# Kernel tuning notes

Hardware: AMD Instinct MI355X
Metric: run time of the kernel (lower is better)

Reference implementation:

```python
import jax, jax.numpy as jnp
import numpy as np

TEMPERATURE = 0.07
BASE_TEMPERATURE = 0.07
EPS = 0.0001  # matches the +0.0001 in the torch code


def _l2norm(x):
    return x / jnp.clip(jnp.linalg.norm(x, axis=-1, keepdims=True), 1e-12, None)


def setup_inputs() -> dict:
    key = jax.random.key(0)
    k1, k2, k3 = jax.random.split(key, 3)
    # Sampled hard anchors: [total_classes=102, n_view=10, d=256], unit-norm
    # (original normalizes feats with F.normalize before _hard_anchor_sampling).
    X_anchor = _l2norm(jax.random.normal(k1, (102, 10, 256), dtype=jnp.float32))
    y_anchor = jax.random.randint(k2, (102,), 0, 19)
    # Memory queue of negatives: [class_num=19, cache_size=5000, d=256], unit-norm.
    queue = _l2norm(jax.random.normal(k3, (19, 5000, 256), dtype=jnp.float32))
    return {"X_anchor": X_anchor, "y_anchor": y_anchor, "queue": queue}


def reference(X_anchor, y_anchor, queue):
    anchor_num, n_view, d = X_anchor.shape
    class_num, cache_size, _ = queue.shape

    # anchor_feature = cat(unbind(X_anchor, dim=1), dim=0)  -> view-major order [n_view*anchor_num, d]
    anchor_feature = jnp.transpose(X_anchor, (1, 0, 2)).reshape(n_view * anchor_num, d)
    # _sample_negative flattens the queue class-major: [class_num*cache_size, d]
    contrast_feature = queue.reshape(class_num * cache_size, d)

    # mask = eq(y_anchor, y_contrast.T) then .repeat(anchor_count=n_view, contrast_count=1)
    y_a = jnp.tile(y_anchor, n_view)                                  # [N]
    y_c = jnp.repeat(jnp.arange(class_num, dtype=y_anchor.dtype), cache_size)  # [M]
    mask = (y_a[:, None] == y_c[None, :]).astype(X_anchor.dtype)      # [N, M]

    logits = jnp.matmul(anchor_feature, contrast_feature.T) / TEMPERATURE  # [N, M]
    logits_max = jax.lax.stop_gradient(jnp.max(logits, axis=1, keepdims=True))
    logits = logits - logits_max

    exp_logits = jnp.exp(logits)
    neg_sum = jnp.sum(exp_logits * (1.0 - mask), axis=1, keepdims=True)  # [N, 1]
    log_prob = logits - jnp.log(exp_logits + neg_sum)

    mean_log_prob_pos = jnp.sum(mask * log_prob, axis=1) / (jnp.sum(mask, axis=1) + EPS)
    loss = -(TEMPERATURE / BASE_TEMPERATURE) * mean_log_prob_pos
    return jnp.mean(loss)
```

## Files before the change

### kernel.cpp

```cpp
#include <hip/hip_runtime.h>
#include <hip/hip_bf16.h>
#include <stdint.h>

#define NCLS   19
#define CACHE  5000
#define NTILE  313
#define DDIM   256
#define NANCH  102
#define NVIEW  10
#define NROWS  1020
#define NSUB   13
#define NCHUNK (NCLS*NSUB)
#define NWG    (4*NCHUNK)
#define SCALE_A 20.6099319733f
#define LN2     0.69314718056f

using bf16x8 = __attribute__((ext_vector_type(8))) __bf16;
using f32x4  = __attribute__((ext_vector_type(4))) float;

#if __has_builtin(__builtin_amdgcn_exp2f)
#define EXP2(x) __builtin_amdgcn_exp2f(x)
#else
#define EXP2(x) __expf((x) * LN2)
#endif

static __device__ __forceinline__ unsigned short f2bf(float x) {
    unsigned int u = __float_as_uint(x);
    unsigned int r = (u + 0x7FFFu + ((u >> 16) & 1u)) >> 16;
    return (unsigned short)r;
}

__global__ __launch_bounds__(256) void conv_anchor2(const float* __restrict__ X,
                                                    unsigned short* __restrict__ Abf) {
    int n = blockIdx.x;
    int k = threadIdx.x;
    float v = 0.f;
    if (n < NROWS) {
        int vv = n / NANCH, a = n - vv * NANCH;
        v = X[((size_t)a * NVIEW + vv) * DDIM + k] * SCALE_A;
    }
    Abf[(size_t)n * DDIM + k] = f2bf(v);
}

__global__ __launch_bounds__(256, 2) void pass1_kernel(
    const unsigned short* __restrict__ Abf, const float* __restrict__ Qf,
    const int* __restrict__ y,
    float* __restrict__ Pt, float* __restrict__ Pe, float* __restrict__ Ps)
{
    __shared__ unsigned char lds[2][8192];

    int orig = blockIdx.x;
    int xcd = orig & 7, slot = orig >> 3;
    int wid = (xcd < 4 ? xcd * 124 : 496 + (xcd - 4) * 123) + slot;
    int rt = wid & 3;
    int cs = wid >> 2;
    int cls = cs / NSUB;
    int sub = cs - cls * NSUB;
    int t0 = (NTILE * sub) / NSUB, t1 = (NTILE * (sub + 1)) / NSUB;

    int tid = threadIdx.x;
    int wave = tid >> 6, lane = tid & 63;
    int lg = lane >> 4, lm = lane & 15;
    int wrb = rt * 256 + wave * 64;

    int c   = tid >> 4;
    int seg = tid & 15;
    int skk = seg >> 1;
    int sidx0 = skk * 64 + ((seg & 1) * 2) * 16 + c;
    unsigned sb0 = (unsigned)(sidx0 * 16) ^ (unsigned)(skk << 4);
    unsigned sb1 = (unsigned)((sidx0 + 16) * 16) ^ (unsigned)(skk << 4);
    const float* qbase = Qf + (size_t)cls * CACHE * DDIM + seg * 16;

    bf16x8 afrag[4][8];
    #pragma unroll
    for (int f = 0; f < 4; ++f)
        #pragma unroll
        for (int kk = 0; kk < 8; ++kk)
            afrag[f][kk] = *reinterpret_cast<const bf16x8*>(
                Abf + (size_t)(wrb + f * 16 + lm) * DDIM + kk * 32 + lg * 8);

    float tacc[4][4] = {}, sacc[4][4] = {};

#define SLOAD(t) do {                                                         \
        int _col = (t) * 16 + c;                                              \
        s_ok = _col < CACHE;                                                  \
        const f32x4* _src = reinterpret_cast<const f32x4*>(                   \
            qbase + (size_t)(s_ok ? _col : CACHE - 1) * DDIM);                \
        s_r0 = _src[0]; s_r1 = _src[1]; s_r2 = _src[2]; s_r3 = _src[3];       \
    } while (0)

#define CVTWRITE(buf) do {                                                    \
        bf16x8 _p0, _p1;                                                      \
        _Pragma("unroll")                                                     \
        for (int j = 0; j < 4; ++j) {                                         \
            _p0[j]     = (__bf16)s_r0[j];                                     \
            _p0[j + 4] = (__bf16)s_r1[j];                                     \
            _p1[j]     = (__bf16)s_r2[j];                                     \
            _p1[j + 4] = (__bf16)s_r3[j];                                     \
        }                                                                     \
        bf16x8 _z = {};                                                       \
        if (!s_ok) { _p0 = _z; _p1 = _z; }                                    \
        *reinterpret_cast<bf16x8*>(&lds[buf][sb0]) = _p0;                     \
        *reinterpret_cast<bf16x8*>(&lds[buf][sb1]) = _p1;                     \
    } while (0)

#define COMPUTE(buf) do {                                                     \
        bf16x8 bfrag[8];                                                      \
        _Pragma("unroll")                                                     \
        for (int kk = 0; kk < 8; ++kk)                                        \
            bfrag[kk] = *reinterpret_cast<const bf16x8*>(                     \
                &lds[buf][(unsigned)((kk * 64 + lane) * 16) ^ (unsigned)(kk << 4)]); \
        f32x4 acc[4];                                                         \
        _Pragma("unroll")                                                     \
        for (int f = 0; f < 4; ++f) acc[f] = (f32x4){0.f, 0.f, 0.f, 0.f};     \
        _Pragma("unroll")                                                     \
        for (int kk = 0; kk < 8; ++kk)                                        \
            _Pragma("unroll")                                                 \
            for (int f = 0; f < 4; ++f)                                       \
                acc[f] = __builtin_amdgcn_mfma_f32_16x16x32_bf16(             \
                    afrag[f][kk], bfrag[kk], acc[f], 0, 0, 0);                \
        _Pragma("unroll")                                                     \
        for (int f = 0; f < 4; ++f)                                           \
            _Pragma("unroll")                                                 \
            for (int r = 0; r < 4; ++r) {                                     \
                float v = acc[f][r];                         \
                tacc[f][r] += EXP2(v);              \
                sacc[f][r] += v;                                              \
            }                                                                 \
    } while (0)

    f32x4 s_r0, s_r1, s_r2, s_r3;
    bool s_ok;
    int nt = t1 - t0;

    SLOAD(t0);
    CVTWRITE(0);
    __syncthreads();

    int cur = 0;
    for (int it = 0; it < nt; ++it) {
        if (it + 1 < nt) SLOAD(t0 + it + 1);
        COMPUTE(cur);
        if (it + 1 < nt) CVTWRITE(cur ^ 1);
        __syncthreads();
        cur ^= 1;
    }
#undef SLOAD
#undef CVTWRITE
#undef COMPUTE

    #pragma unroll
    for (int f = 0; f < 4; ++f)
        #pragma unroll
        for (int r = 0; r < 4; ++r) {
            float t = tacc[f][r], s = sacc[f][r];
            #pragma unroll
            for (int m = 1; m < 16; m <<= 1) {
                t += __shfl_xor(t, m);
                s += __shfl_xor(s, m);
            }
            if (lm == 0) {
                int row = wrb + f * 16 + lg * 4 + r;
                float mp = (row < NROWS && y[row % NANCH] == cls) ? 1.0f : 0.0f;
                size_t idx = (size_t)cs * 1024 + row;
                Pt[idx] = t; Pe[idx] = mp * t; Ps[idx] = mp * s;
            }
        }
}

__global__ __launch_bounds__(256) void reduce_rows(const float* __restrict__ Pt,
                                                   const float* __restrict__ Pe,
                                                   const float* __restrict__ Ps,
                                                   float* __restrict__ rowloss) {
    int tid = threadIdx.x;
    int row = blockIdx.x * 64 + (tid >> 2);
    int part = tid & 3;
    float tot = 0.f, pe = 0.f, ps = 0.f;
    for (int c = part; c < NCHUNK; c += 4) {
        size_t idx = (size_t)c * 1024 + row;
        tot += Pt[idx]; pe += Pe[idx]; ps += Ps[idx];
    }
    tot += __shfl_xor(tot, 1); pe += __shfl_xor(pe, 1); ps += __shfl_xor(ps, 1);
    tot += __shfl_xor(tot, 2); pe += __shfl_xor(pe, 2); ps += __shfl_xor(ps, 2);
    if (part == 0) {
        float r = 0.f;
        if (row < NROWS) {
            float ns    = tot - pe - 144.0f;
            float pos_e = pe - 8.0f;
            float pos_s = ps * LN2;
            float sum_logprob = pos_s - (5000.0f * logf(ns) + pos_e / ns);
            r = -sum_logprob / (5000.0f + 1e-4f);
        }
        rowloss[row] = r;
    }
}

__global__ __launch_bounds__(256) void pass3_kernel(const float* __restrict__ rowloss,
                                                    float* __restrict__ out) {
    float local = 0.f;
    for (int n = threadIdx.x; n < 1024; n += 256) local += rowloss[n];
    #pragma unroll
    for (int m = 1; m < 64; m <<= 1) local += __shfl_xor(local, m);
    __shared__ float sb[4];
    if ((threadIdx.x & 63) == 0) sb[threadIdx.x >> 6] = local;
    __syncthreads();
    if (threadIdx.x == 0)
        out[0] = (sb[0] + sb[1] + sb[2] + sb[3]) * (1.0f / (float)NROWS);
}

extern "C" void kernel_launch(void* const* d_in, const int* in_sizes, int n_in,
                              void* d_out, int out_size, void* d_ws, size_t ws_size,
                              hipStream_t stream) {
    const float* X  = (const float*)d_in[0];
    const int*   y  = (const int*)d_in[1];
    const float* Qf = (const float*)d_in[2];
    float* out = (float*)d_out;

    char* ws = (char*)d_ws;
    unsigned short* Abf = (unsigned short*)(ws);
    float* Pt      = (float*)(ws + 524288);
    float* Pe      = (float*)(ws + 1536000);
    float* Ps      = (float*)(ws + 2547712);
    float* rowloss = (float*)(ws + 3559424);

    conv_anchor2<<<1024, 256, 0, stream>>>(X, Abf);
    pass1_kernel<<<NWG, 256, 0, stream>>>(Abf, Qf, y, Pt, Pe, Ps);
    reduce_rows<<<16, 256, 0, stream>>>(Pt, Pe, Ps, rowloss);
    pass3_kernel<<<1, 256, 0, stream>>>(rowloss, out);
}
```

Before: 103.3 us.

## Split anchor rows into 8 row tiles per chunk and simplify LDS layout

Doubles the workgroup count by splitting the 1024 anchor rows into 8 tiles of 128 rather than 4 of 256. Each wave now holds 2 A fragments instead of 4, which cuts register pressure enough to raise launch bounds to 3 workgroups per SIMD. The staging thread mapping is changed to row-major, and the XOR-swizzled LDS layout is dropped in favour of plain offsets. The aim is more occupancy and parallelism to hide latency, at the cost of each queue tile being loaded and converted twice as often and possible LDS bank conflicts.

```diff
diff --git a/kernel.cpp b/kernel.cpp
--- a/kernel.cpp
+++ b/kernel.cpp
@@ -11,7 +11,7 @@
 #define NROWS  1020
 #define NSUB   13
 #define NCHUNK (NCLS*NSUB)
-#define NWG    (4*NCHUNK)
+#define NWG    (8*NCHUNK)
 #define SCALE_A 20.6099319733f
 #define LN2     0.69314718056f
 
@@ -42,7 +42,7 @@
     Abf[(size_t)n * DDIM + k] = f2bf(v);
 }
 
-__global__ __launch_bounds__(256, 2) void pass1_kernel(
+__global__ __launch_bounds__(256, 3) void pass1_kernel(
     const unsigned short* __restrict__ Abf, const float* __restrict__ Qf,
     const int* __restrict__ y,
     float* __restrict__ Pt, float* __restrict__ Pe, float* __restrict__ Ps)
@@ -51,9 +51,9 @@
 
     int orig = blockIdx.x;
     int xcd = orig & 7, slot = orig >> 3;
-    int wid = (xcd < 4 ? xcd * 124 : 496 + (xcd - 4) * 123) + slot;
-    int rt = wid & 3;
-    int cs = wid >> 2;
+    int wid = xcd * 247 + slot;
+    int rt = wid & 7;
+    int cs = wid >> 3;
     int cls = cs / NSUB;
     int sub = cs - cls * NSUB;
     int t0 = (NTILE * sub) / NSUB, t1 = (NTILE * (sub + 1)) / NSUB;
@@ -61,25 +61,21 @@
     int tid = threadIdx.x;
     int wave = tid >> 6, lane = tid & 63;
     int lg = lane >> 4, lm = lane & 15;
-    int wrb = rt * 256 + wave * 64;
-
-    int c   = tid >> 4;
-    int seg = tid & 15;
-    int skk = seg >> 1;
-    int sidx0 = skk * 64 + ((seg & 1) * 2) * 16 + c;
-    unsigned sb0 = (unsigned)(sidx0 * 16) ^ (unsigned)(skk << 4);
-    unsigned sb1 = (unsigned)((sidx0 + 16) * 16) ^ (unsigned)(skk << 4);
-    const float* qbase = Qf + (size_t)cls * CACHE * DDIM + seg * 16;
-
-    bf16x8 afrag[4][8];
+    int wrb = rt * 128 + wave * 32;
+
+    int c = tid & 15, r = tid >> 4;
+    unsigned wb0 = (unsigned)((r >> 1) * 1024 + (r & 1) * 512 + c * 16);
+    const float* qbase = Qf + (size_t)cls * CACHE * DDIM + r * 16;
+
+    bf16x8 afrag[2][8];
     #pragma unroll
-    for (int f = 0; f < 4; ++f)
+    for (int f = 0; f < 2; ++f)
         #pragma unroll
         for (int kk = 0; kk < 8; ++kk)
             afrag[f][kk] = *reinterpret_cast<const bf16x8*>(
                 Abf + (size_t)(wrb + f * 16 + lm) * DDIM + kk * 32 + lg * 8);
 
-    float tacc[4][4] = {}, sacc[4][4] = {};
+    float tacc[2][4] = {}, sacc[2][4] = {};
 
 #define SLOAD(t) do {                                                         \
         int _col = (t) * 16 + c;                                              \
@@ -100,8 +96,8 @@
         }                                                                     \
         bf16x8 _z = {};                                                       \
         if (!s_ok) { _p0 = _z; _p1 = _z; }                                    \
-        *reinterpret_cast<bf16x8*>(&lds[buf][sb0]) = _p0;                     \
-        *reinterpret_cast<bf16x8*>(&lds[buf][sb1]) = _p1;                     \
+        *reinterpret_cast<bf16x8*>(&lds[buf][wb0])       = _p0;               \
+        *reinterpret_cast<bf16x8*>(&lds[buf][wb0 + 256]) = _p1;               \
     } while (0)
 
 #define COMPUTE(buf) do {                                                     \
@@ -109,24 +105,21 @@
         _Pragma("unroll")                                                     \
         for (int kk = 0; kk < 8; ++kk)                                        \
             bfrag[kk] = *reinterpret_cast<const bf16x8*>(                     \
-                &lds[buf][(unsigned)((kk * 64 + lane) * 16) ^ (unsigned)(kk << 4)]); \
-        f32x4 acc[4];                                                         \
-        _Pragma("unroll")                                                     \
-        for (int f = 0; f < 4; ++f) acc[f] = (f32x4){0.f, 0.f, 0.f, 0.f};     \
-        _Pragma("unroll")                                                     \
-        for (int kk = 0; kk < 8; ++kk)                                        \
-            _Pragma("unroll")                                                 \
-            for (int f = 0; f < 4; ++f)                                       \
-                acc[f] = __builtin_amdgcn_mfma_f32_16x16x32_bf16(             \
-                    afrag[f][kk], bfrag[kk], acc[f], 0, 0, 0);                \
-        _Pragma("unroll")                                                     \
-        for (int f = 0; f < 4; ++f)                                           \
-            _Pragma("unroll")                                                 \
-            for (int r = 0; r < 4; ++r) {                                     \
-                float v = acc[f][r];                         \
-                tacc[f][r] += EXP2(v);              \
-                sacc[f][r] += v;                                              \
-            }                                                                 \
+                &lds[buf][(kk * 64 + lane) * 16]);                            \
+        f32x4 acc0 = {0.f,0.f,0.f,0.f}, acc1 = {0.f,0.f,0.f,0.f};             \
+        _Pragma("unroll")                                                     \
+        for (int kk = 0; kk < 8; ++kk) {                                      \
+            acc0 = __builtin_amdgcn_mfma_f32_16x16x32_bf16(                   \
+                afrag[0][kk], bfrag[kk], acc0, 0, 0, 0);                      \
+            acc1 = __builtin_amdgcn_mfma_f32_16x16x32_bf16(                   \
+                afrag[1][kk], bfrag[kk], acc1, 0, 0, 0);                      \
+        }                                                                     \
+        _Pragma("unroll")                                                     \
+        for (int r_ = 0; r_ < 4; ++r_) {                                      \
+            float v0 = acc0[r_], v1 = acc1[r_];                               \
+            tacc[0][r_] += EXP2(v0);  sacc[0][r_] += v0;                      \
+            tacc[1][r_] += EXP2(v1);  sacc[1][r_] += v1;                      \
+        }                                                                     \
     } while (0)
 
     f32x4 s_r0, s_r1, s_r2, s_r3;
@@ -150,17 +143,17 @@
 #undef COMPUTE
 
     #pragma unroll
-    for (int f = 0; f < 4; ++f)
+    for (int f = 0; f < 2; ++f)
         #pragma unroll
-        for (int r = 0; r < 4; ++r) {
-            float t = tacc[f][r], s = sacc[f][r];
+        for (int r_ = 0; r_ < 4; ++r_) {
+            float t = tacc[f][r_], s = sacc[f][r_];
             #pragma unroll
             for (int m = 1; m < 16; m <<= 1) {
                 t += __shfl_xor(t, m);
                 s += __shfl_xor(s, m);
             }
             if (lm == 0) {
-                int row = wrb + f * 16 + lg * 4 + r;
+                int row = wrb + f * 16 + lg * 4 + r_;
                 float mp = (row < NROWS && y[row % NANCH] == cls) ? 1.0f : 0.0f;
                 size_t idx = (size_t)cs * 1024 + row;
                 Pt[idx] = t; Pe[idx] = mp * t; Ps[idx] = mp * s;
```

New measurement: 142.9 us. 38.3% more time.

## Compute positive logit sums via class column-sums and use 512-thread workgroups

Applied to the files above, without the earlier changes.

Removes the per-element accumulation of raw logits in the main GEMM loop. The positive-logit sum is now computed algebraically as the dot product of each anchor row with its class's column sum of queue vectors, accumulated during staging and combined in a new small kernel. Workgroups grow to 512 threads covering 512 rows, which halves the grid and the number of times each queue tile is reloaded from global memory. The LDS swizzle is dropped, which may introduce bank conflicts. The colsum is taken over fp32 values rather than bf16, so rounding differs slightly from before.

```diff
diff --git a/kernel.cpp b/kernel.cpp
--- a/kernel.cpp
+++ b/kernel.cpp
@@ -11,7 +11,7 @@
 #define NROWS  1020
 #define NSUB   13
 #define NCHUNK (NCLS*NSUB)
-#define NWG    (4*NCHUNK)
+#define NWG    (2*NCHUNK)
 #define SCALE_A 20.6099319733f
 #define LN2     0.69314718056f
 
@@ -42,18 +42,18 @@
     Abf[(size_t)n * DDIM + k] = f2bf(v);
 }
 
-__global__ __launch_bounds__(256, 2) void pass1_kernel(
+__global__ __launch_bounds__(512, 1) void pass1_kernel(
     const unsigned short* __restrict__ Abf, const float* __restrict__ Qf,
     const int* __restrict__ y,
-    float* __restrict__ Pt, float* __restrict__ Pe, float* __restrict__ Ps)
+    float* __restrict__ Pt, float* __restrict__ Pe, float* __restrict__ Pcs)
 {
     __shared__ unsigned char lds[2][8192];
 
     int orig = blockIdx.x;
     int xcd = orig & 7, slot = orig >> 3;
-    int wid = (xcd < 4 ? xcd * 124 : 496 + (xcd - 4) * 123) + slot;
-    int rt = wid & 3;
-    int cs = wid >> 2;
+    int wid = (xcd < 6 ? xcd * 62 : 372 + (xcd - 6) * 61) + slot;
+    int rt = wid & 1;
+    int cs = wid >> 1;
     int cls = cs / NSUB;
     int sub = cs - cls * NSUB;
     int t0 = (NTILE * sub) / NSUB, t1 = (NTILE * (sub + 1)) / NSUB;
@@ -61,15 +61,13 @@
     int tid = threadIdx.x;
     int wave = tid >> 6, lane = tid & 63;
     int lg = lane >> 4, lm = lane & 15;
-    int wrb = rt * 256 + wave * 64;
-
-    int c   = tid >> 4;
-    int seg = tid & 15;
-    int skk = seg >> 1;
-    int sidx0 = skk * 64 + ((seg & 1) * 2) * 16 + c;
-    unsigned sb0 = (unsigned)(sidx0 * 16) ^ (unsigned)(skk << 4);
-    unsigned sb1 = (unsigned)((sidx0 + 16) * 16) ^ (unsigned)(skk << 4);
-    const float* qbase = Qf + (size_t)cls * CACHE * DDIM + seg * 16;
+    int wrb = rt * 512 + wave * 64;
+
+    int c = tid & 15, r = tid >> 4;
+    unsigned wb = (unsigned)(((r >> 2) * 64 + (r & 3) * 16 + c) * 16);
+    const float* qbase = Qf + (size_t)cls * CACHE * DDIM + r * 8;
+    bool docs = (rt == 0);
+    float csum[8] = {};
 
     bf16x8 afrag[4][8];
     #pragma unroll
@@ -79,29 +77,34 @@
             afrag[f][kk] = *reinterpret_cast<const bf16x8*>(
                 Abf + (size_t)(wrb + f * 16 + lm) * DDIM + kk * 32 + lg * 8);
 
-    float tacc[4][4] = {}, sacc[4][4] = {};
+    float tacc[4][4] = {};
 
 #define SLOAD(t) do {                                                         \
         int _col = (t) * 16 + c;                                              \
         s_ok = _col < CACHE;                                                  \
         const f32x4* _src = reinterpret_cast<const f32x4*>(                   \
             qbase + (size_t)(s_ok ? _col : CACHE - 1) * DDIM);                \
-        s_r0 = _src[0]; s_r1 = _src[1]; s_r2 = _src[2]; s_r3 = _src[3];       \
+        s_r0 = _src[0]; s_r1 = _src[1];                                       \
     } while (0)
 
 #define CVTWRITE(buf) do {                                                    \
-        bf16x8 _p0, _p1;                                                      \
+        bf16x8 _p;                                                            \
         _Pragma("unroll")                                                     \
         for (int j = 0; j < 4; ++j) {                                         \
-            _p0[j]     = (__bf16)s_r0[j];                                     \
-            _p0[j + 4] = (__bf16)s_r1[j];                                     \
-            _p1[j]     = (__bf16)s_r2[j];                                     \
-            _p1[j + 4] = (__bf16)s_r3[j];                                     \
+            _p[j]     = (__bf16)s_r0[j];                                      \
+            _p[j + 4] = (__bf16)s_r1[j];                                      \
         }                                                                     \
-        bf16x8 _z = {};                                                       \
-        if (!s_ok) { _p0 = _z; _p1 = _z; }                                    \
-        *reinterpret_cast<bf16x8*>(&lds[buf][sb0]) = _p0;                     \
-        *reinterpret_cast<bf16x8*>(&lds[buf][sb1]) = _p1;                     \
+        if (!s_ok) {                                                          \
+            bf16x8 _z = {};                                                   \
+            _p = _z;                                                          \
+        } else if (docs) {                                                    \
+            _Pragma("unroll")                                                 \
+            for (int j = 0; j < 4; ++j) {                                     \
+                csum[j]     += s_r0[j];                                       \
+                csum[j + 4] += s_r1[j];                                       \
+            }                                                                 \
+        }                                                                     \
+        *reinterpret_cast<bf16x8*>(&lds[buf][wb]) = _p;                       \
     } while (0)
 
 #define COMPUTE(buf) do {                                                     \
@@ -109,7 +112,7 @@
         _Pragma("unroll")                                                     \
         for (int kk = 0; kk < 8; ++kk)                                        \
             bfrag[kk] = *reinterpret_cast<const bf16x8*>(                     \
-                &lds[buf][(unsigned)((kk * 64 + lane) * 16) ^ (unsigned)(kk << 4)]); \
+                &lds[buf][(kk * 64 + lane) * 16]);                            \
         f32x4 acc[4];                                                         \
         _Pragma("unroll")                                                     \
         for (int f = 0; f < 4; ++f) acc[f] = (f32x4){0.f, 0.f, 0.f, 0.f};     \
@@ -122,14 +125,11 @@
         _Pragma("unroll")                                                     \
         for (int f = 0; f < 4; ++f)                                           \
             _Pragma("unroll")                                                 \
-            for (int r = 0; r < 4; ++r) {                                     \
-                float v = acc[f][r];                         \
-                tacc[f][r] += EXP2(v);              \
-                sacc[f][r] += v;                                              \
-            }                                                                 \
+            for (int r_ = 0; r_ < 4; ++r_)                                    \
+                tacc[f][r_] += EXP2(acc[f][r_]);    \
     } while (0)
 
-    f32x4 s_r0, s_r1, s_r2, s_r3;
+    f32x4 s_r0, s_r1;
     bool s_ok;
     int nt = t1 - t0;
 
@@ -152,46 +152,82 @@
     #pragma unroll
     for (int f = 0; f < 4; ++f)
         #pragma unroll
-        for (int r = 0; r < 4; ++r) {
-            float t = tacc[f][r], s = sacc[f][r];
+        for (int r_ = 0; r_ < 4; ++r_) {
+            float t = tacc[f][r_];
             #pragma unroll
-            for (int m = 1; m < 16; m <<= 1) {
-                t += __shfl_xor(t, m);
-                s += __shfl_xor(s, m);
-            }
+            for (int m = 1; m < 16; m <<= 1) t += __shfl_xor(t, m);
             if (lm == 0) {
-                int row = wrb + f * 16 + lg * 4 + r;
+                int row = wrb + f * 16 + lg * 4 + r_;
                 float mp = (row < NROWS && y[row % NANCH] == cls) ? 1.0f : 0.0f;
                 size_t idx = (size_t)cs * 1024 + row;
-                Pt[idx] = t; Pe[idx] = mp * t; Ps[idx] = mp * s;
+                Pt[idx] = t; Pe[idx] = mp * t;
             }
         }
+
+    if (docs) {
+        #pragma unroll
+        for (int j = 0; j < 8; ++j) {
+            float v = csum[j];
+            v += __shfl_xor(v, 1);
+            v += __shfl_xor(v, 2);
+            v += __shfl_xor(v, 4);
+            v += __shfl_xor(v, 8);
+            if (c == 0) Pcs[(size_t)cs * DDIM + r * 8 + j] = v;
+        }
+    }
+}
+
+__global__ __launch_bounds__(256) void colsum_combine(const float* __restrict__ Pcs,
+                                                      float* __restrict__ colsum) {
+    int cls = blockIdx.x, k = threadIdx.x;
+    float s = 0.f;
+    for (int sub = 0; sub < NSUB; ++sub)
+        s += Pcs[(size_t)(cls * NSUB + sub) * DDIM + k];
+    colsum[cls * DDIM + k] = s;
 }
 
 __global__ __launch_bounds__(256) void reduce_rows(const float* __restrict__ Pt,
                                                    const float* __restrict__ Pe,
-                                                   const float* __restrict__ Ps,
+                                                   const float* __restrict__ colsum,
+                                                   const unsigned short* __restrict__ Abf,
+                                                   const int* __restrict__ y,
                                                    float* __restrict__ rowloss) {
     int tid = threadIdx.x;
     int row = blockIdx.x * 64 + (tid >> 2);
     int part = tid & 3;
-    float tot = 0.f, pe = 0.f, ps = 0.f;
-    for (int c = part; c < NCHUNK; c += 4) {
-        size_t idx = (size_t)c * 1024 + row;
-        tot += Pt[idx]; pe += Pe[idx]; ps += Ps[idx];
-    }
-    tot += __shfl_xor(tot, 1); pe += __shfl_xor(pe, 1); ps += __shfl_xor(ps, 1);
-    tot += __shfl_xor(tot, 2); pe += __shfl_xor(pe, 2); ps += __shfl_xor(ps, 2);
+    float tot = 0.f, pe = 0.f;
+    for (int cc = part; cc < NCHUNK; cc += 4) {
+        size_t idx = (size_t)cc * 1024 + row;
+        tot += Pt[idx]; pe += Pe[idx];
+    }
+    float psd = 0.f;
+    if (row < NROWS) {
+        int cls = y[row % NANCH];
+        const bf16x8* arow = reinterpret_cast<const bf16x8*>(
+            Abf + (size_t)row * DDIM) + part * 8;
+        const f32x4* csp = reinterpret_cast<const f32x4*>(
+            colsum + cls * DDIM + part * 64);
+        #pragma unroll
+        for (int i = 0; i < 8; ++i) {
+            bf16x8 av = arow[i];
+            f32x4 c0 = csp[i * 2], c1 = csp[i * 2 + 1];
+            #pragma unroll
+            for (int j = 0; j < 4; ++j)
+                psd += (float)av[j] * c0[j] + (float)av[j + 4] * c1[j];
+        }
+    }
+    tot += __shfl_xor(tot, 1); pe += __shfl_xor(pe, 1); psd += __shfl_xor(psd, 1);
+    tot += __shfl_xor(tot, 2); pe += __shfl_xor(pe, 2); psd += __shfl_xor(psd, 2);
     if (part == 0) {
-        float r = 0.f;
+        float rl = 0.f;
         if (row < NROWS) {
             float ns    = tot - pe - 144.0f;
             float pos_e = pe - 8.0f;
-            float pos_s = ps * LN2;
+            float pos_s = psd * LN2;
             float sum_logprob = pos_s - (5000.0f * logf(ns) + pos_e / ns);
-            r = -sum_logprob / (5000.0f + 1e-4f);
-        }
-        rowloss[row] = r;
+            rl = -sum_logprob / (5000.0f + 1e-4f);
+        }
+        rowloss[row] = rl;
     }
 }
 
@@ -220,11 +256,13 @@
     unsigned short* Abf = (unsigned short*)(ws);
     float* Pt      = (float*)(ws + 524288);
     float* Pe      = (float*)(ws + 1536000);
-    float* Ps      = (float*)(ws + 2547712);
-    float* rowloss = (float*)(ws + 3559424);
+    float* Pcs     = (float*)(ws + 2547712);
+    float* colsum  = (float*)(ws + 2800640);
+    float* rowloss = (float*)(ws + 2820096);
 
     conv_anchor2<<<1024, 256, 0, stream>>>(X, Abf);
-    pass1_kernel<<<NWG, 256, 0, stream>>>(Abf, Qf, y, Pt, Pe, Ps);
-    reduce_rows<<<16, 256, 0, stream>>>(Pt, Pe, Ps, rowloss);
+    pass1_kernel<<<NWG, 512, 0, stream>>>(Abf, Qf, y, Pt, Pe, Pcs);
+    colsum_combine<<<NCLS, 256, 0, stream>>>(Pcs, colsum);
+    reduce_rows<<<16, 256, 0, stream>>>(Pt, Pe, colsum, Abf, y, rowloss);
     pass3_kernel<<<1, 256, 0, stream>>>(rowloss, out);
 }
```

Measured after the change: 111.2 us. 7.6% more time.
